# Optimization experiments

Measured on AMD Instinct MI355X. Metric: run time of the kernel, lower is better.

Reference implementation:

```python
import jax, jax.numpy as jnp
import numpy as np

N_NODES = 100000
N_EDGES = 2000000
D_IN = 4
HID = 64


def setup_inputs() -> dict:
    key = jax.random.key(0)
    ks = jax.random.split(key, 8)
    node_feats = jax.random.normal(ks[0], (N_NODES, D_IN), dtype=jnp.float32)
    pairs = jax.random.randint(ks[1], (N_EDGES, 2), 0, N_NODES, dtype=jnp.int64)
    # Kaiming-ish init scaling
    W1 = jax.random.normal(ks[2], (D_IN, HID), dtype=jnp.float32) / np.sqrt(D_IN)
    b1 = jnp.zeros((HID,), dtype=jnp.float32)
    W2 = jax.random.normal(ks[3], (HID, HID), dtype=jnp.float32) / np.sqrt(HID)
    b2 = jnp.zeros((HID,), dtype=jnp.float32)
    We1 = jax.random.normal(ks[4], (3 * HID, HID), dtype=jnp.float32) / np.sqrt(3 * HID)
    be1 = jnp.zeros((HID,), dtype=jnp.float32)
    We2 = jax.random.normal(ks[5], (HID, 1), dtype=jnp.float32) / np.sqrt(HID)
    be2 = jnp.zeros((1,), dtype=jnp.float32)
    return {"node_feats": node_feats, "pairs": pairs, "W1": W1, "b1": b1,
            "W2": W2, "b2": b2, "We1": We1, "be1": be1, "We2": We2, "be2": be2}


def reference(node_feats, pairs, W1, b1, W2, b2, We1, be1, We2, be2):
    # node MLP: Linear -> ReLU -> Linear -> ReLU
    H = jax.nn.relu(node_feats @ W1 + b1)      # [N, HID]
    H = jax.nn.relu(H @ W2 + b2)               # [N, HID]
    # vectorized gather over all edge pairs (replaces Python loop)
    hu = H[pairs[:, 0]]                        # [E, HID]
    hv = H[pairs[:, 1]]                        # [E, HID]
    E = jnp.concatenate([hu, hv, jnp.abs(hu - hv)], axis=-1)  # [E, 3*HID]
    # edge MLP: Linear -> ReLU -> Linear, squeeze last dim
    scores = (jax.nn.relu(E @ We1 + be1) @ We2 + be2)[:, 0]   # [E]
    return scores
```

## Files before the change

### kernel.cpp

```cpp
#include <hip/hip_runtime.h>

#define N_NODES 100000
#define N_EDGES 2000000

typedef __bf16 bf16x8 __attribute__((ext_vector_type(8)));
typedef float f32x4 __attribute__((ext_vector_type(4)));

__device__ __forceinline__ unsigned f2bf_rne(float f) {
  unsigned u = __builtin_bit_cast(unsigned, f);
  u += 0x7FFFu + ((u >> 16) & 1u);
  return u >> 16;
}

__device__ __forceinline__ unsigned pack_rhu(float lo, float hi) {
  unsigned ulo = __builtin_bit_cast(unsigned, lo) + 0x8000u;
  unsigned uhi = __builtin_bit_cast(unsigned, hi) + 0x8000u;
  return __builtin_amdgcn_perm(uhi, ulo, 0x07060302u);
}

__device__ __forceinline__ unsigned absdiff_pack(unsigned a, unsigned b) {
  float alo = __builtin_bit_cast(float, a << 16);
  float ahi = __builtin_bit_cast(float, a & 0xFFFF0000u);
  float blo = __builtin_bit_cast(float, b << 16);
  float bhi = __builtin_bit_cast(float, b & 0xFFFF0000u);
  return pack_rhu(fabsf(alo - blo), fabsf(ahi - bhi));
}

__global__ __launch_bounds__(64) void node_mfma_kernel(
    const float* __restrict__ X, const float* __restrict__ W1,
    const float* __restrict__ b1, const float* __restrict__ W2,
    const float* __restrict__ b2, unsigned short* __restrict__ H) {
  const int lane = threadIdx.x;
  const int l15 = lane & 15;
  const int quad = lane >> 4;

  float w1v[2][4][8], b1v[2][8];
#pragma unroll
  for (int c = 0; c < 2; ++c)
#pragma unroll
    for (int j = 0; j < 8; ++j) {
      int col = c * 32 + quad * 8 + j;
      b1v[c][j] = b1[col];
#pragma unroll
      for (int d = 0; d < 4; ++d) w1v[c][d][j] = W1[d * 64 + col];
    }

  uint4 afr[2][4];
#pragma unroll
  for (int c = 0; c < 2; ++c)
#pragma unroll
    for (int mt = 0; mt < 4; ++mt) {
      unsigned w[4];
#pragma unroll
      for (int p = 0; p < 4; ++p) {
        int k = c * 32 + quad * 8 + 2 * p;
        unsigned lo = f2bf_rne(W2[k * 64 + mt * 16 + l15]);
        unsigned hi = f2bf_rne(W2[(k + 1) * 64 + mt * 16 + l15]);
        w[p] = lo | (hi << 16);
      }
      afr[c][mt] = make_uint4(w[0], w[1], w[2], w[3]);
    }
  float b2v[16];
#pragma unroll
  for (int mt = 0; mt < 4; ++mt)
#pragma unroll
    for (int r = 0; r < 4; ++r) b2v[mt * 4 + r] = b2[mt * 16 + quad * 4 + r];

  const int tile = blockIdx.x;
  float4 xv = ((const float4*)X)[tile * 16 + l15];

  uint4 bfr[2];
#pragma unroll
  for (int c = 0; c < 2; ++c) {
    unsigned w[4];
#pragma unroll
    for (int p = 0; p < 4; ++p) {
      float h0 = fmaxf(b1v[c][2 * p] + xv.x * w1v[c][0][2 * p] +
                           xv.y * w1v[c][1][2 * p] + xv.z * w1v[c][2][2 * p] +
                           xv.w * w1v[c][3][2 * p],
                       0.f);
      float h1 = fmaxf(b1v[c][2 * p + 1] + xv.x * w1v[c][0][2 * p + 1] +
                           xv.y * w1v[c][1][2 * p + 1] +
                           xv.z * w1v[c][2][2 * p + 1] +
                           xv.w * w1v[c][3][2 * p + 1],
                       0.f);
      w[p] = pack_rhu(h0, h1);
    }
    bfr[c] = make_uint4(w[0], w[1], w[2], w[3]);
  }

  f32x4 acc[4];
#pragma unroll
  for (int mt = 0; mt < 4; ++mt) acc[mt] = (f32x4){0.f, 0.f, 0.f, 0.f};
#pragma unroll
  for (int c = 0; c < 2; ++c)
#pragma unroll
    for (int mt = 0; mt < 4; ++mt)
      acc[mt] = __builtin_amdgcn_mfma_f32_16x16x32_bf16(
          __builtin_bit_cast(bf16x8, afr[c][mt]),
          __builtin_bit_cast(bf16x8, bfr[c]), acc[mt], 0, 0, 0);

  unsigned short* hrow = H + (tile * 16 + l15) * 64;
#pragma unroll
  for (int mt = 0; mt < 4; ++mt) {
    unsigned lo = pack_rhu(fmaxf(acc[mt][0] + b2v[mt * 4 + 0], 0.f),
                           fmaxf(acc[mt][1] + b2v[mt * 4 + 1], 0.f));
    unsigned hi = pack_rhu(fmaxf(acc[mt][2] + b2v[mt * 4 + 2], 0.f),
                           fmaxf(acc[mt][3] + b2v[mt * 4 + 3], 0.f));
    *(uint2*)(hrow + mt * 16 + quad * 4) = make_uint2(lo, hi);
  }
}

__global__ __launch_bounds__(256, 2) void edge_mlp_kernel(
    const unsigned short* __restrict__ H, const int* __restrict__ pairs,
    const float* __restrict__ We1, const float* __restrict__ be1,
    const float* __restrict__ We2, const float* __restrict__ be2,
    float* __restrict__ out) {
  const int tid = threadIdx.x;
  const int lane = tid & 63;
  const int l15 = lane & 15;
  const int quad = lane >> 4;

  uint4 afr[6][4];
#pragma unroll
  for (int c = 0; c < 6; ++c)
#pragma unroll
    for (int mt = 0; mt < 4; ++mt) {
      unsigned w[4];
#pragma unroll
      for (int p = 0; p < 4; ++p) {
        int k = c * 32 + quad * 8 + 2 * p;
        unsigned lo = f2bf_rne(We1[k * 64 + mt * 16 + l15]);
        unsigned hi = f2bf_rne(We1[(k + 1) * 64 + mt * 16 + l15]);
        w[p] = lo | (hi << 16);
      }
      afr[c][mt] = make_uint4(w[0], w[1], w[2], w[3]);
    }
  float be1v[16], we2v[16];
#pragma unroll
  for (int mt = 0; mt < 4; ++mt)
#pragma unroll
    for (int r = 0; r < 4; ++r) {
      be1v[mt * 4 + r] = be1[mt * 16 + quad * 4 + r];
      we2v[mt * 4 + r] = We2[mt * 16 + quad * 4 + r];
    }
  const float be2v = be2[0];

  const int wid = blockIdx.x * 4 + (tid >> 6);
  const int nw = gridDim.x * 4;
  const int ntiles = N_EDGES / 16;
  const int2* pairs2 = (const int2*)pairs;

  int t1 = wid + nw;
  int2 uvA = pairs2[wid * 16 + l15];
  int2 uvB = pairs2[(t1 < ntiles ? t1 : wid) * 16 + l15];
  const uint4* pu = (const uint4*)(H + uvA.x * 64 + quad * 8);
  const uint4* pv = (const uint4*)(H + uvA.y * 64 + quad * 8);
  uint4 g0 = pu[0], g1 = pu[4], g2 = pv[0], g3 = pv[4];

  for (int tile = wid; tile < ntiles; tile += nw) {
    const uint4* qu = (const uint4*)(H + uvB.x * 64 + quad * 8);
    const uint4* qv = (const uint4*)(H + uvB.y * 64 + quad * 8);
    uint4 n0 = qu[0], n1 = qu[4], n2 = qv[0], n3 = qv[4];
    int t2 = tile + 2 * nw;
    int2 uvC = pairs2[(t2 < ntiles ? t2 : tile) * 16 + l15];

    uint4 ab0, ab1;
    ab0.x = absdiff_pack(g0.x, g2.x);
    ab0.y = absdiff_pack(g0.y, g2.y);
    ab0.z = absdiff_pack(g0.z, g2.z);
    ab0.w = absdiff_pack(g0.w, g2.w);
    ab1.x = absdiff_pack(g1.x, g3.x);
    ab1.y = absdiff_pack(g1.y, g3.y);
    ab1.z = absdiff_pack(g1.z, g3.z);
    ab1.w = absdiff_pack(g1.w, g3.w);

    bf16x8 b[6];
    b[0] = __builtin_bit_cast(bf16x8, g0);
    b[1] = __builtin_bit_cast(bf16x8, g1);
    b[2] = __builtin_bit_cast(bf16x8, g2);
    b[3] = __builtin_bit_cast(bf16x8, g3);
    b[4] = __builtin_bit_cast(bf16x8, ab0);
    b[5] = __builtin_bit_cast(bf16x8, ab1);

    f32x4 acc[4];
#pragma unroll
    for (int mt = 0; mt < 4; ++mt) acc[mt] = (f32x4){0.f, 0.f, 0.f, 0.f};
#pragma unroll
    for (int c = 0; c < 6; ++c)
#pragma unroll
      for (int mt = 0; mt < 4; ++mt)
        acc[mt] = __builtin_amdgcn_mfma_f32_16x16x32_bf16(
            __builtin_bit_cast(bf16x8, afr[c][mt]), b[c], acc[mt], 0, 0, 0);

    float s = 0.f;
#pragma unroll
    for (int mt = 0; mt < 4; ++mt)
#pragma unroll
      for (int r = 0; r < 4; ++r)
        s += fmaxf(acc[mt][r] + be1v[mt * 4 + r], 0.f) * we2v[mt * 4 + r];
    s += __shfl_xor(s, 16);
    s += __shfl_xor(s, 32);
    if (quad == 0) out[tile * 16 + l15] = s + be2v;

    g0 = n0;
    g1 = n1;
    g2 = n2;
    g3 = n3;
    uvB = uvC;
  }
}

extern "C" void kernel_launch(void* const* d_in, const int* in_sizes, int n_in,
                              void* d_out, int out_size, void* d_ws,
                              size_t ws_size, hipStream_t stream) {
  const float* X = (const float*)d_in[0];
  const int* pairs = (const int*)d_in[1];
  const float* W1 = (const float*)d_in[2];
  const float* b1 = (const float*)d_in[3];
  const float* W2 = (const float*)d_in[4];
  const float* b2 = (const float*)d_in[5];
  const float* We1 = (const float*)d_in[6];
  const float* be1 = (const float*)d_in[7];
  const float* We2 = (const float*)d_in[8];
  const float* be2 = (const float*)d_in[9];
  float* out = (float*)d_out;
  unsigned short* H = (unsigned short*)d_ws;

  node_mfma_kernel<<<N_NODES / 16, 64, 0, stream>>>(X, W1, b1, W2, b2, H);
  edge_mlp_kernel<<<1024, 256, 0, stream>>>(H, pairs, We1, be1, We2, be2, out);
}
```

Baseline: 183.2 us.

## Deepen edge gather prefetch to two tiles and make node kernel grid-stride

The edge kernel now keeps two tiles of gathered H rows in flight instead of one, with index loads running three tiles ahead, to hide random-gather latency. The node kernel switches from one block per 16-node tile to a persistent grid of 1024 blocks that loop over tiles, amortizing the per-block weight loading and bf16 conversion of W1/W2. The deeper prefetch raises register pressure in the edge kernel, which could lower occupancy under the (256,2) bound. The node kernel's fixed 1024-block grid of 64-thread blocks may underfill the GPU.

```diff
diff --git a/kernel.cpp b/kernel.cpp
--- a/kernel.cpp
+++ b/kernel.cpp
@@ -26,7 +26,7 @@
   return pack_rhu(fabsf(alo - blo), fabsf(ahi - bhi));
 }
 
-__global__ __launch_bounds__(64) void node_mfma_kernel(
+__global__ __launch_bounds__(64, 1) void node_mfma_kernel(
     const float* __restrict__ X, const float* __restrict__ W1,
     const float* __restrict__ b1, const float* __restrict__ W2,
     const float* __restrict__ b2, unsigned short* __restrict__ H) {
@@ -66,48 +66,50 @@
 #pragma unroll
     for (int r = 0; r < 4; ++r) b2v[mt * 4 + r] = b2[mt * 16 + quad * 4 + r];
 
-  const int tile = blockIdx.x;
-  float4 xv = ((const float4*)X)[tile * 16 + l15];
-
-  uint4 bfr[2];
-#pragma unroll
-  for (int c = 0; c < 2; ++c) {
-    unsigned w[4];
-#pragma unroll
-    for (int p = 0; p < 4; ++p) {
-      float h0 = fmaxf(b1v[c][2 * p] + xv.x * w1v[c][0][2 * p] +
-                           xv.y * w1v[c][1][2 * p] + xv.z * w1v[c][2][2 * p] +
-                           xv.w * w1v[c][3][2 * p],
-                       0.f);
-      float h1 = fmaxf(b1v[c][2 * p + 1] + xv.x * w1v[c][0][2 * p + 1] +
-                           xv.y * w1v[c][1][2 * p + 1] +
-                           xv.z * w1v[c][2][2 * p + 1] +
-                           xv.w * w1v[c][3][2 * p + 1],
-                       0.f);
-      w[p] = pack_rhu(h0, h1);
-    }
-    bfr[c] = make_uint4(w[0], w[1], w[2], w[3]);
-  }
-
-  f32x4 acc[4];
-#pragma unroll
-  for (int mt = 0; mt < 4; ++mt) acc[mt] = (f32x4){0.f, 0.f, 0.f, 0.f};
-#pragma unroll
-  for (int c = 0; c < 2; ++c)
-#pragma unroll
-    for (int mt = 0; mt < 4; ++mt)
-      acc[mt] = __builtin_amdgcn_mfma_f32_16x16x32_bf16(
-          __builtin_bit_cast(bf16x8, afr[c][mt]),
-          __builtin_bit_cast(bf16x8, bfr[c]), acc[mt], 0, 0, 0);
-
-  unsigned short* hrow = H + (tile * 16 + l15) * 64;
-#pragma unroll
-  for (int mt = 0; mt < 4; ++mt) {
-    unsigned lo = pack_rhu(fmaxf(acc[mt][0] + b2v[mt * 4 + 0], 0.f),
-                           fmaxf(acc[mt][1] + b2v[mt * 4 + 1], 0.f));
-    unsigned hi = pack_rhu(fmaxf(acc[mt][2] + b2v[mt * 4 + 2], 0.f),
-                           fmaxf(acc[mt][3] + b2v[mt * 4 + 3], 0.f));
-    *(uint2*)(hrow + mt * 16 + quad * 4) = make_uint2(lo, hi);
+  const int ntiles = N_NODES / 16;
+  for (int tile = blockIdx.x; tile < ntiles; tile += gridDim.x) {
+    float4 xv = ((const float4*)X)[tile * 16 + l15];
+
+    uint4 bfr[2];
+#pragma unroll
+    for (int c = 0; c < 2; ++c) {
+      unsigned w[4];
+#pragma unroll
+      for (int p = 0; p < 4; ++p) {
+        float h0 = fmaxf(b1v[c][2 * p] + xv.x * w1v[c][0][2 * p] +
+                             xv.y * w1v[c][1][2 * p] + xv.z * w1v[c][2][2 * p] +
+                             xv.w * w1v[c][3][2 * p],
+                         0.f);
+        float h1 = fmaxf(b1v[c][2 * p + 1] + xv.x * w1v[c][0][2 * p + 1] +
+                             xv.y * w1v[c][1][2 * p + 1] +
+                             xv.z * w1v[c][2][2 * p + 1] +
+                             xv.w * w1v[c][3][2 * p + 1],
+                         0.f);
+        w[p] = pack_rhu(h0, h1);
+      }
+      bfr[c] = make_uint4(w[0], w[1], w[2], w[3]);
+    }
+
+    f32x4 acc[4];
+#pragma unroll
+    for (int mt = 0; mt < 4; ++mt) acc[mt] = (f32x4){0.f, 0.f, 0.f, 0.f};
+#pragma unroll
+    for (int c = 0; c < 2; ++c)
+#pragma unroll
+      for (int mt = 0; mt < 4; ++mt)
+        acc[mt] = __builtin_amdgcn_mfma_f32_16x16x32_bf16(
+            __builtin_bit_cast(bf16x8, afr[c][mt]),
+            __builtin_bit_cast(bf16x8, bfr[c]), acc[mt], 0, 0, 0);
+
+    unsigned short* hrow = H + (tile * 16 + l15) * 64;
+#pragma unroll
+    for (int mt = 0; mt < 4; ++mt) {
+      unsigned lo = pack_rhu(fmaxf(acc[mt][0] + b2v[mt * 4 + 0], 0.f),
+                             fmaxf(acc[mt][1] + b2v[mt * 4 + 1], 0.f));
+      unsigned hi = pack_rhu(fmaxf(acc[mt][2] + b2v[mt * 4 + 2], 0.f),
+                             fmaxf(acc[mt][3] + b2v[mt * 4 + 3], 0.f));
+      *(uint2*)(hrow + mt * 16 + quad * 4) = make_uint2(lo, hi);
+    }
   }
 }
 
@@ -151,19 +153,23 @@
   const int ntiles = N_EDGES / 16;
   const int2* pairs2 = (const int2*)pairs;
 
-  int t1 = wid + nw;
-  int2 uvA = pairs2[wid * 16 + l15];
-  int2 uvB = pairs2[(t1 < ntiles ? t1 : wid) * 16 + l15];
-  const uint4* pu = (const uint4*)(H + uvA.x * 64 + quad * 8);
-  const uint4* pv = (const uint4*)(H + uvA.y * 64 + quad * 8);
+  int t1 = wid + nw, t2 = wid + 2 * nw;
+  int2 uv0 = pairs2[wid * 16 + l15];
+  int2 uv1 = pairs2[(t1 < ntiles ? t1 : wid) * 16 + l15];
+  int2 uv2 = pairs2[(t2 < ntiles ? t2 : wid) * 16 + l15];
+  const uint4* pu = (const uint4*)(H + uv0.x * 64 + quad * 8);
+  const uint4* pv = (const uint4*)(H + uv0.y * 64 + quad * 8);
   uint4 g0 = pu[0], g1 = pu[4], g2 = pv[0], g3 = pv[4];
+  const uint4* ru = (const uint4*)(H + uv1.x * 64 + quad * 8);
+  const uint4* rv = (const uint4*)(H + uv1.y * 64 + quad * 8);
+  uint4 h0 = ru[0], h1 = ru[4], h2 = rv[0], h3 = rv[4];
 
   for (int tile = wid; tile < ntiles; tile += nw) {
-    const uint4* qu = (const uint4*)(H + uvB.x * 64 + quad * 8);
-    const uint4* qv = (const uint4*)(H + uvB.y * 64 + quad * 8);
-    uint4 n0 = qu[0], n1 = qu[4], n2 = qv[0], n3 = qv[4];
-    int t2 = tile + 2 * nw;
-    int2 uvC = pairs2[(t2 < ntiles ? t2 : tile) * 16 + l15];
+    const uint4* qu = (const uint4*)(H + uv2.x * 64 + quad * 8);
+    const uint4* qv = (const uint4*)(H + uv2.y * 64 + quad * 8);
+    uint4 i0 = qu[0], i1 = qu[4], i2 = qv[0], i3 = qv[4];
+    int t3 = tile + 3 * nw;
+    int2 uvn = pairs2[(t3 < ntiles ? t3 : tile) * 16 + l15];
 
     uint4 ab0, ab1;
     ab0.x = absdiff_pack(g0.x, g2.x);
@@ -203,11 +209,9 @@
     s += __shfl_xor(s, 32);
     if (quad == 0) out[tile * 16 + l15] = s + be2v;
 
-    g0 = n0;
-    g1 = n1;
-    g2 = n2;
-    g3 = n3;
-    uvB = uvC;
+    g0 = h0; g1 = h1; g2 = h2; g3 = h3;
+    h0 = i0; h1 = i1; h2 = i2; h3 = i3;
+    uv2 = uvn;
   }
 }
 
@@ -227,6 +231,6 @@
   float* out = (float*)d_out;
   unsigned short* H = (unsigned short*)d_ws;
 
-  node_mfma_kernel<<<N_NODES / 16, 64, 0, stream>>>(X, W1, b1, W2, b2, H);
+  node_mfma_kernel<<<1024, 64, 0, stream>>>(X, W1, b1, W2, b2, H);
   edge_mlp_kernel<<<1024, 256, 0, stream>>>(H, pairs, We1, be1, We2, be2, out);
 }
```

Result: no change. 183.0 us (-0.1%).

## Stage edge weights in LDS for occupancy; make node kernel grid-stride

Applied to the files above, without the earlier changes.

The edge kernel no longer keeps all 24 We1 weight fragments in registers. Each block converts them to bf16 once, stores them in shared memory, and each wave reads them from LDS before every MFMA. This frees VGPRs so launch bounds can allow 3 blocks per SM instead of 2, giving more waves to hide gather latency, at the cost of extra LDS reads in the inner loop. The node kernel becomes a grid-stride loop over 1024 blocks, so weight setup is amortized across tiles instead of repeated for every tile.

```diff
diff --git a/kernel.cpp b/kernel.cpp
--- a/kernel.cpp
+++ b/kernel.cpp
@@ -26,7 +26,7 @@
   return pack_rhu(fabsf(alo - blo), fabsf(ahi - bhi));
 }
 
-__global__ __launch_bounds__(64) void node_mfma_kernel(
+__global__ __launch_bounds__(64, 1) void node_mfma_kernel(
     const float* __restrict__ X, const float* __restrict__ W1,
     const float* __restrict__ b1, const float* __restrict__ W2,
     const float* __restrict__ b2, unsigned short* __restrict__ H) {
@@ -66,76 +66,82 @@
 #pragma unroll
     for (int r = 0; r < 4; ++r) b2v[mt * 4 + r] = b2[mt * 16 + quad * 4 + r];
 
-  const int tile = blockIdx.x;
-  float4 xv = ((const float4*)X)[tile * 16 + l15];
-
-  uint4 bfr[2];
-#pragma unroll
-  for (int c = 0; c < 2; ++c) {
-    unsigned w[4];
-#pragma unroll
-    for (int p = 0; p < 4; ++p) {
-      float h0 = fmaxf(b1v[c][2 * p] + xv.x * w1v[c][0][2 * p] +
-                           xv.y * w1v[c][1][2 * p] + xv.z * w1v[c][2][2 * p] +
-                           xv.w * w1v[c][3][2 * p],
-                       0.f);
-      float h1 = fmaxf(b1v[c][2 * p + 1] + xv.x * w1v[c][0][2 * p + 1] +
-                           xv.y * w1v[c][1][2 * p + 1] +
-                           xv.z * w1v[c][2][2 * p + 1] +
-                           xv.w * w1v[c][3][2 * p + 1],
-                       0.f);
-      w[p] = pack_rhu(h0, h1);
-    }
-    bfr[c] = make_uint4(w[0], w[1], w[2], w[3]);
+  const int ntiles = N_NODES / 16;
+  for (int tile = blockIdx.x; tile < ntiles; tile += gridDim.x) {
+    float4 xv = ((const float4*)X)[tile * 16 + l15];
+
+    uint4 bfr[2];
+#pragma unroll
+    for (int c = 0; c < 2; ++c) {
+      unsigned w[4];
+#pragma unroll
+      for (int p = 0; p < 4; ++p) {
+        float h0 = fmaxf(b1v[c][2 * p] + xv.x * w1v[c][0][2 * p] +
+                             xv.y * w1v[c][1][2 * p] + xv.z * w1v[c][2][2 * p] +
+                             xv.w * w1v[c][3][2 * p],
+                         0.f);
+        float h1 = fmaxf(b1v[c][2 * p + 1] + xv.x * w1v[c][0][2 * p + 1] +
+                             xv.y * w1v[c][1][2 * p + 1] +
+                             xv.z * w1v[c][2][2 * p + 1] +
+                             xv.w * w1v[c][3][2 * p + 1],
+                         0.f);
+        w[p] = pack_rhu(h0, h1);
+      }
+      bfr[c] = make_uint4(w[0], w[1], w[2], w[3]);
+    }
+
+    f32x4 acc[4];
+#pragma unroll
+    for (int mt = 0; mt < 4; ++mt) acc[mt] = (f32x4){0.f, 0.f, 0.f, 0.f};
+#pragma unroll
+    for (int c = 0; c < 2; ++c)
+#pragma unroll
+      for (int mt = 0; mt < 4; ++mt)
+        acc[mt] = __builtin_amdgcn_mfma_f32_16x16x32_bf16(
+            __builtin_bit_cast(bf16x8, afr[c][mt]),
+            __builtin_bit_cast(bf16x8, bfr[c]), acc[mt], 0, 0, 0);
+
+    unsigned short* hrow = H + (tile * 16 + l15) * 64;
+#pragma unroll
+    for (int mt = 0; mt < 4; ++mt) {
+      unsigned lo = pack_rhu(fmaxf(acc[mt][0] + b2v[mt * 4 + 0], 0.f),
+                             fmaxf(acc[mt][1] + b2v[mt * 4 + 1], 0.f));
+      unsigned hi = pack_rhu(fmaxf(acc[mt][2] + b2v[mt * 4 + 2], 0.f),
+                             fmaxf(acc[mt][3] + b2v[mt * 4 + 3], 0.f));
+      *(uint2*)(hrow + mt * 16 + quad * 4) = make_uint2(lo, hi);
+    }
   }
-
-  f32x4 acc[4];
-#pragma unroll
-  for (int mt = 0; mt < 4; ++mt) acc[mt] = (f32x4){0.f, 0.f, 0.f, 0.f};
-#pragma unroll
-  for (int c = 0; c < 2; ++c)
-#pragma unroll
-    for (int mt = 0; mt < 4; ++mt)
-      acc[mt] = __builtin_amdgcn_mfma_f32_16x16x32_bf16(
-          __builtin_bit_cast(bf16x8, afr[c][mt]),
-          __builtin_bit_cast(bf16x8, bfr[c]), acc[mt], 0, 0, 0);
-
-  unsigned short* hrow = H + (tile * 16 + l15) * 64;
-#pragma unroll
-  for (int mt = 0; mt < 4; ++mt) {
-    unsigned lo = pack_rhu(fmaxf(acc[mt][0] + b2v[mt * 4 + 0], 0.f),
-                           fmaxf(acc[mt][1] + b2v[mt * 4 + 1], 0.f));
-    unsigned hi = pack_rhu(fmaxf(acc[mt][2] + b2v[mt * 4 + 2], 0.f),
-                           fmaxf(acc[mt][3] + b2v[mt * 4 + 3], 0.f));
-    *(uint2*)(hrow + mt * 16 + quad * 4) = make_uint2(lo, hi);
-  }
-}
-
-__global__ __launch_bounds__(256, 2) void edge_mlp_kernel(
+}
+
+__global__ __launch_bounds__(256, 3) void edge_mlp_kernel(
     const unsigned short* __restrict__ H, const int* __restrict__ pairs,
     const float* __restrict__ We1, const float* __restrict__ be1,
     const float* __restrict__ We2, const float* __restrict__ be2,
     float* __restrict__ out) {
+  __shared__ uint4 wlds[1536];
   const int tid = threadIdx.x;
+
+  for (int s = tid; s < 1536; s += 256) {
+    int f = s >> 6;
+    int ln = s & 63;
+    int c = f >> 2, mt = f & 3;
+    int kb = c * 32 + (ln >> 4) * 8;
+    int col = mt * 16 + (ln & 15);
+    unsigned w0 = f2bf_rne(We1[(kb + 0) * 64 + col]) |
+                  (f2bf_rne(We1[(kb + 1) * 64 + col]) << 16);
+    unsigned w1 = f2bf_rne(We1[(kb + 2) * 64 + col]) |
+                  (f2bf_rne(We1[(kb + 3) * 64 + col]) << 16);
+    unsigned w2 = f2bf_rne(We1[(kb + 4) * 64 + col]) |
+                  (f2bf_rne(We1[(kb + 5) * 64 + col]) << 16);
+    unsigned w3 = f2bf_rne(We1[(kb + 6) * 64 + col]) |
+                  (f2bf_rne(We1[(kb + 7) * 64 + col]) << 16);
+    wlds[s] = make_uint4(w0, w1, w2, w3);
+  }
+
   const int lane = tid & 63;
   const int l15 = lane & 15;
   const int quad = lane >> 4;
 
-  uint4 afr[6][4];
-#pragma unroll
-  for (int c = 0; c < 6; ++c)
-#pragma unroll
-    for (int mt = 0; mt < 4; ++mt) {
-      unsigned w[4];
-#pragma unroll
-      for (int p = 0; p < 4; ++p) {
-        int k = c * 32 + quad * 8 + 2 * p;
-        unsigned lo = f2bf_rne(We1[k * 64 + mt * 16 + l15]);
-        unsigned hi = f2bf_rne(We1[(k + 1) * 64 + mt * 16 + l15]);
-        w[p] = lo | (hi << 16);
-      }
-      afr[c][mt] = make_uint4(w[0], w[1], w[2], w[3]);
-    }
   float be1v[16], we2v[16];
 #pragma unroll
   for (int mt = 0; mt < 4; ++mt)
@@ -145,11 +151,13 @@
       we2v[mt * 4 + r] = We2[mt * 16 + quad * 4 + r];
     }
   const float be2v = be2[0];
+  __syncthreads();
 
   const int wid = blockIdx.x * 4 + (tid >> 6);
   const int nw = gridDim.x * 4;
   const int ntiles = N_EDGES / 16;
   const int2* pairs2 = (const int2*)pairs;
+  const uint4* wfrag = wlds + lane;
 
   int t1 = wid + nw;
   int2 uvA = pairs2[wid * 16 + l15];
@@ -189,9 +197,11 @@
 #pragma unroll
     for (int c = 0; c < 6; ++c)
 #pragma unroll
-      for (int mt = 0; mt < 4; ++mt)
-        acc[mt] = __builtin_amdgcn_mfma_f32_16x16x32_bf16(
-            __builtin_bit_cast(bf16x8, afr[c][mt]), b[c], acc[mt], 0, 0, 0);
+      for (int mt = 0; mt < 4; ++mt) {
+        bf16x8 a = __builtin_bit_cast(bf16x8, wfrag[(c * 4 + mt) * 64]);
+        acc[mt] =
+            __builtin_amdgcn_mfma_f32_16x16x32_bf16(a, b[c], acc[mt], 0, 0, 0);
+      }
 
     float s = 0.f;
 #pragma unroll
@@ -227,6 +237,6 @@
   float* out = (float*)d_out;
   unsigned short* H = (unsigned short*)d_ws;
 
-  node_mfma_kernel<<<N_NODES / 16, 64, 0, stream>>>(X, W1, b1, W2, b2, H);
+  node_mfma_kernel<<<1024, 64, 0, stream>>>(X, W1, b1, W2, b2, H);
   edge_mlp_kernel<<<1024, 256, 0, stream>>>(H, pairs, We1, be1, We2, be2, out);
 }
```

New measurement: 265.1 us. +44.7%, slower.

## Split edge MLP hidden columns across wave pairs and combine with atomics

Applied to the files above, without the earlier changes.

Each 16-edge tile is now handled by two waves, each computing half of the 64 hidden columns, so every wave keeps half the weight fragments in registers. This should allow three blocks per SM instead of two. The partial scores are combined with atomicAdd into an output that the node kernel zero-fills first. The node kernel also becomes persistent with a grid-stride loop over tiles. In exchange, every edge's H rows are gathered twice (once per wave) and atomic traffic is added to the output.

```diff
diff --git a/kernel.cpp b/kernel.cpp
--- a/kernel.cpp
+++ b/kernel.cpp
@@ -26,10 +26,19 @@
   return pack_rhu(fabsf(alo - blo), fabsf(ahi - bhi));
 }
 
-__global__ __launch_bounds__(64) void node_mfma_kernel(
+__global__ __launch_bounds__(64, 1) void node_mfma_kernel(
     const float* __restrict__ X, const float* __restrict__ W1,
     const float* __restrict__ b1, const float* __restrict__ W2,
-    const float* __restrict__ b2, unsigned short* __restrict__ H) {
+    const float* __restrict__ b2, unsigned short* __restrict__ H,
+    float* __restrict__ out) {
+  {
+    float4 z = {0.f, 0.f, 0.f, 0.f};
+    float4* o4 = (float4*)out;
+    for (int i = blockIdx.x * 64 + threadIdx.x; i < N_EDGES / 4;
+         i += gridDim.x * 64)
+      o4[i] = z;
+  }
+
   const int lane = threadIdx.x;
   const int l15 = lane & 15;
   const int quad = lane >> 4;
@@ -66,52 +75,54 @@
 #pragma unroll
     for (int r = 0; r < 4; ++r) b2v[mt * 4 + r] = b2[mt * 16 + quad * 4 + r];
 
-  const int tile = blockIdx.x;
-  float4 xv = ((const float4*)X)[tile * 16 + l15];
-
-  uint4 bfr[2];
-#pragma unroll
-  for (int c = 0; c < 2; ++c) {
-    unsigned w[4];
-#pragma unroll
-    for (int p = 0; p < 4; ++p) {
-      float h0 = fmaxf(b1v[c][2 * p] + xv.x * w1v[c][0][2 * p] +
-                           xv.y * w1v[c][1][2 * p] + xv.z * w1v[c][2][2 * p] +
-                           xv.w * w1v[c][3][2 * p],
-                       0.f);
-      float h1 = fmaxf(b1v[c][2 * p + 1] + xv.x * w1v[c][0][2 * p + 1] +
-                           xv.y * w1v[c][1][2 * p + 1] +
-                           xv.z * w1v[c][2][2 * p + 1] +
-                           xv.w * w1v[c][3][2 * p + 1],
-                       0.f);
-      w[p] = pack_rhu(h0, h1);
-    }
-    bfr[c] = make_uint4(w[0], w[1], w[2], w[3]);
+  const int ntiles = N_NODES / 16;
+  for (int tile = blockIdx.x; tile < ntiles; tile += gridDim.x) {
+    float4 xv = ((const float4*)X)[tile * 16 + l15];
+
+    uint4 bfr[2];
+#pragma unroll
+    for (int c = 0; c < 2; ++c) {
+      unsigned w[4];
+#pragma unroll
+      for (int p = 0; p < 4; ++p) {
+        float h0 = fmaxf(b1v[c][2 * p] + xv.x * w1v[c][0][2 * p] +
+                             xv.y * w1v[c][1][2 * p] + xv.z * w1v[c][2][2 * p] +
+                             xv.w * w1v[c][3][2 * p],
+                         0.f);
+        float h1 = fmaxf(b1v[c][2 * p + 1] + xv.x * w1v[c][0][2 * p + 1] +
+                             xv.y * w1v[c][1][2 * p + 1] +
+                             xv.z * w1v[c][2][2 * p + 1] +
+                             xv.w * w1v[c][3][2 * p + 1],
+                         0.f);
+        w[p] = pack_rhu(h0, h1);
+      }
+      bfr[c] = make_uint4(w[0], w[1], w[2], w[3]);
+    }
+
+    f32x4 acc[4];
+#pragma unroll
+    for (int mt = 0; mt < 4; ++mt) acc[mt] = (f32x4){0.f, 0.f, 0.f, 0.f};
+#pragma unroll
+    for (int c = 0; c < 2; ++c)
+#pragma unroll
+      for (int mt = 0; mt < 4; ++mt)
+        acc[mt] = __builtin_amdgcn_mfma_f32_16x16x32_bf16(
+            __builtin_bit_cast(bf16x8, afr[c][mt]),
+            __builtin_bit_cast(bf16x8, bfr[c]), acc[mt], 0, 0, 0);
+
+    unsigned short* hrow = H + (tile * 16 + l15) * 64;
+#pragma unroll
+    for (int mt = 0; mt < 4; ++mt) {
+      unsigned lo = pack_rhu(fmaxf(acc[mt][0] + b2v[mt * 4 + 0], 0.f),
+                             fmaxf(acc[mt][1] + b2v[mt * 4 + 1], 0.f));
+      unsigned hi = pack_rhu(fmaxf(acc[mt][2] + b2v[mt * 4 + 2], 0.f),
+                             fmaxf(acc[mt][3] + b2v[mt * 4 + 3], 0.f));
+      *(uint2*)(hrow + mt * 16 + quad * 4) = make_uint2(lo, hi);
+    }
   }
-
-  f32x4 acc[4];
-#pragma unroll
-  for (int mt = 0; mt < 4; ++mt) acc[mt] = (f32x4){0.f, 0.f, 0.f, 0.f};
-#pragma unroll
-  for (int c = 0; c < 2; ++c)
-#pragma unroll
-    for (int mt = 0; mt < 4; ++mt)
-      acc[mt] = __builtin_amdgcn_mfma_f32_16x16x32_bf16(
-          __builtin_bit_cast(bf16x8, afr[c][mt]),
-          __builtin_bit_cast(bf16x8, bfr[c]), acc[mt], 0, 0, 0);
-
-  unsigned short* hrow = H + (tile * 16 + l15) * 64;
-#pragma unroll
-  for (int mt = 0; mt < 4; ++mt) {
-    unsigned lo = pack_rhu(fmaxf(acc[mt][0] + b2v[mt * 4 + 0], 0.f),
-                           fmaxf(acc[mt][1] + b2v[mt * 4 + 1], 0.f));
-    unsigned hi = pack_rhu(fmaxf(acc[mt][2] + b2v[mt * 4 + 2], 0.f),
-                           fmaxf(acc[mt][3] + b2v[mt * 4 + 3], 0.f));
-    *(uint2*)(hrow + mt * 16 + quad * 4) = make_uint2(lo, hi);
-  }
-}
-
-__global__ __launch_bounds__(256, 2) void edge_mlp_kernel(
+}
+
+__global__ __launch_bounds__(256, 3) void edge_mlp_kernel(
     const unsigned short* __restrict__ H, const int* __restrict__ pairs,
     const float* __restrict__ We1, const float* __restrict__ be1,
     const float* __restrict__ We2, const float* __restrict__ be2,
@@ -120,49 +131,52 @@
   const int lane = tid & 63;
   const int l15 = lane & 15;
   const int quad = lane >> 4;
-
-  uint4 afr[6][4];
+  const int mth = (tid >> 6) & 1;
+
+  uint4 afr[6][2];
 #pragma unroll
   for (int c = 0; c < 6; ++c)
 #pragma unroll
-    for (int mt = 0; mt < 4; ++mt) {
+    for (int jt = 0; jt < 2; ++jt) {
+      int col = (mth * 2 + jt) * 16 + l15;
       unsigned w[4];
 #pragma unroll
       for (int p = 0; p < 4; ++p) {
         int k = c * 32 + quad * 8 + 2 * p;
-        unsigned lo = f2bf_rne(We1[k * 64 + mt * 16 + l15]);
-        unsigned hi = f2bf_rne(We1[(k + 1) * 64 + mt * 16 + l15]);
+        unsigned lo = f2bf_rne(We1[k * 64 + col]);
+        unsigned hi = f2bf_rne(We1[(k + 1) * 64 + col]);
         w[p] = lo | (hi << 16);
       }
-      afr[c][mt] = make_uint4(w[0], w[1], w[2], w[3]);
-    }
-  float be1v[16], we2v[16];
-#pragma unroll
-  for (int mt = 0; mt < 4; ++mt)
+      afr[c][jt] = make_uint4(w[0], w[1], w[2], w[3]);
+    }
+  float be1v[8], we2v[8];
+#pragma unroll
+  for (int jt = 0; jt < 2; ++jt)
 #pragma unroll
     for (int r = 0; r < 4; ++r) {
-      be1v[mt * 4 + r] = be1[mt * 16 + quad * 4 + r];
-      we2v[mt * 4 + r] = We2[mt * 16 + quad * 4 + r];
-    }
-  const float be2v = be2[0];
-
-  const int wid = blockIdx.x * 4 + (tid >> 6);
-  const int nw = gridDim.x * 4;
+      int row = (mth * 2 + jt) * 16 + quad * 4 + r;
+      be1v[jt * 4 + r] = be1[row];
+      we2v[jt * 4 + r] = We2[row];
+    }
+  const float be2h = (mth == 0) ? be2[0] : 0.f;
+
+  const int pid = blockIdx.x * 2 + (tid >> 7);
+  const int np = gridDim.x * 2;
   const int ntiles = N_EDGES / 16;
   const int2* pairs2 = (const int2*)pairs;
 
-  int t1 = wid + nw;
-  int2 uvA = pairs2[wid * 16 + l15];
-  int2 uvB = pairs2[(t1 < ntiles ? t1 : wid) * 16 + l15];
+  int t1 = pid + np;
+  int2 uvA = pairs2[pid * 16 + l15];
+  int2 uvB = pairs2[(t1 < ntiles ? t1 : pid) * 16 + l15];
   const uint4* pu = (const uint4*)(H + uvA.x * 64 + quad * 8);
   const uint4* pv = (const uint4*)(H + uvA.y * 64 + quad * 8);
   uint4 g0 = pu[0], g1 = pu[4], g2 = pv[0], g3 = pv[4];
 
-  for (int tile = wid; tile < ntiles; tile += nw) {
+  for (int tile = pid; tile < ntiles; tile += np) {
     const uint4* qu = (const uint4*)(H + uvB.x * 64 + quad * 8);
     const uint4* qv = (const uint4*)(H + uvB.y * 64 + quad * 8);
     uint4 n0 = qu[0], n1 = qu[4], n2 = qv[0], n3 = qv[4];
-    int t2 = tile + 2 * nw;
+    int t2 = tile + 2 * np;
     int2 uvC = pairs2[(t2 < ntiles ? t2 : tile) * 16 + l15];
 
     uint4 ab0, ab1;
@@ -183,25 +197,25 @@
     b[4] = __builtin_bit_cast(bf16x8, ab0);
     b[5] = __builtin_bit_cast(bf16x8, ab1);
 
-    f32x4 acc[4];
-#pragma unroll
-    for (int mt = 0; mt < 4; ++mt) acc[mt] = (f32x4){0.f, 0.f, 0.f, 0.f};
+    f32x4 acc[2];
+    acc[0] = (f32x4){0.f, 0.f, 0.f, 0.f};
+    acc[1] = (f32x4){0.f, 0.f, 0.f, 0.f};
 #pragma unroll
     for (int c = 0; c < 6; ++c)
 #pragma unroll
-      for (int mt = 0; mt < 4; ++mt)
-        acc[mt] = __builtin_amdgcn_mfma_f32_16x16x32_bf16(
-            __builtin_bit_cast(bf16x8, afr[c][mt]), b[c], acc[mt], 0, 0, 0);
+      for (int jt = 0; jt < 2; ++jt)
+        acc[jt] = __builtin_amdgcn_mfma_f32_16x16x32_bf16(
+            __builtin_bit_cast(bf16x8, afr[c][jt]), b[c], acc[jt], 0, 0, 0);
 
     float s = 0.f;
 #pragma unroll
-    for (int mt = 0; mt < 4; ++mt)
+    for (int jt = 0; jt < 2; ++jt)
 #pragma unroll
       for (int r = 0; r < 4; ++r)
-        s += fmaxf(acc[mt][r] + be1v[mt * 4 + r], 0.f) * we2v[mt * 4 + r];
+        s += fmaxf(acc[jt][r] + be1v[jt * 4 + r], 0.f) * we2v[jt * 4 + r];
     s += __shfl_xor(s, 16);
     s += __shfl_xor(s, 32);
-    if (quad == 0) out[tile * 16 + l15] = s + be2v;
+    if (quad == 0) atomicAdd(&out[tile * 16 + l15], s + be2h);
 
     g0 = n0;
     g1 = n1;
@@ -227,6 +241,6 @@
   float* out = (float*)d_out;
   unsigned short* H = (unsigned short*)d_ws;
 
-  node_mfma_kernel<<<N_NODES / 16, 64, 0, stream>>>(X, W1, b1, W2, b2, H);
-  edge_mlp_kernel<<<1024, 256, 0, stream>>>(H, pairs, We1, be1, We2, be2, out);
-}
+  node_mfma_kernel<<<1024, 64, 0, stream>>>(X, W1, b1, W2, b2, H, out);
+  edge_mlp_kernel<<<768, 256, 0, stream>>>(H, pairs, We1, be1, We2, be2, out);
+}
```

Measured after the change: 219.1 us. 19.6% more time.
